# Kernel tuning notes

Measured on AMD Instinct MI355X. Metric: run time of the kernel, lower is better.

Reference implementation:

```python
import jax, jax.numpy as jnp
import numpy as np

D = 1024      # latent_dimension
NH = 8        # num_heads
ND = 256      # drug num_functions
NT = 128      # target num_functions
B = 128       # batch
EPS_LN = 1e-5
EPS_COS = 1e-8


def _proj_attend(x, W, b, in_w, in_b, out_w, out_b, g, beta):
    """ParallelFcWithAttention.forward: per-feature Linear(1,D)+ReLU, MHSA, LN, sum.
    x: (B, >=F); W,b: (F, D); in_w: (3D, D); out_w: (D, D); g,beta: (D,)."""
    F = W.shape[0]
    # fused batched scale+bias+ReLU replacing the Python loop of Linear(1,D)
    h = jax.nn.relu(x[:, :F, None] * W[None] + b[None])           # (B, F, D)
    Bsz = h.shape[0]
    qkv = h @ in_w.T + in_b                                       # (B, F, 3D)
    q, k, v = jnp.split(qkv, 3, axis=-1)
    Dh = D // NH
    def split_heads(t):
        return t.reshape(Bsz, F, NH, Dh).transpose(0, 2, 1, 3)   # (B, H, F, Dh)
    q, k, v = split_heads(q), split_heads(k), split_heads(v)
    scale = np.float32(1.0 / np.sqrt(Dh))
    scores = jnp.einsum('bhqd,bhkd->bhqk', q, k) * scale          # (B, H, F, F)
    attn = jax.nn.softmax(scores, axis=-1)
    o = jnp.einsum('bhqk,bhkd->bhqd', attn, v)                    # (B, H, F, Dh)
    o = o.transpose(0, 2, 1, 3).reshape(Bsz, F, D)
    o = o @ out_w.T + out_b
    mu = o.mean(axis=-1, keepdims=True)
    var = ((o - mu) ** 2).mean(axis=-1, keepdims=True)
    o = (o - mu) / jnp.sqrt(var + EPS_LN) * g + beta              # LayerNorm
    return o.sum(axis=1)                                          # (B, D)


def setup_inputs() -> dict:
    key = jax.random.key(0)
    ks = jax.random.split(key, 20)
    s = np.float32(0.02)
    inp = {
        'drug':    jax.random.normal(ks[0], (B, 2048), jnp.float32),
        'target':  jax.random.normal(ks[1], (B, 1024), jnp.float32),
        'dW':      jax.random.normal(ks[2], (ND, D), jnp.float32) * s,
        'db':      jax.random.normal(ks[3], (ND, D), jnp.float32) * s,
        'd_in_w':  jax.random.normal(ks[4], (3 * D, D), jnp.float32) * s,
        'd_in_b':  jnp.zeros((3 * D,), jnp.float32),
        'd_out_w': jax.random.normal(ks[5], (D, D), jnp.float32) * s,
        'd_out_b': jnp.zeros((D,), jnp.float32),
        'd_g':     jnp.ones((D,), jnp.float32),
        'd_beta':  jnp.zeros((D,), jnp.float32),
        'tW':      jax.random.normal(ks[6], (NT, D), jnp.float32) * s,
        'tb':      jax.random.normal(ks[7], (NT, D), jnp.float32) * s,
        't_in_w':  jax.random.normal(ks[8], (3 * D, D), jnp.float32) * s,
        't_in_b':  jnp.zeros((3 * D,), jnp.float32),
        't_out_w': jax.random.normal(ks[9], (D, D), jnp.float32) * s,
        't_out_b': jnp.zeros((D,), jnp.float32),
        't_g':     jnp.ones((D,), jnp.float32),
        't_beta':  jnp.zeros((D,), jnp.float32),
    }
    return inp


def reference(drug, target, dW, db, d_in_w, d_in_b, d_out_w, d_out_b, d_g, d_beta,
              tW, tb, t_in_w, t_in_b, t_out_w, t_out_b, t_g, t_beta):
    dp = _proj_attend(drug, dW, db, d_in_w, d_in_b, d_out_w, d_out_b, d_g, d_beta)   # (B, D)
    tp = _proj_attend(target, tW, tb, t_in_w, t_in_b, t_out_w, t_out_b, t_g, t_beta) # (B, D)
    # Cosine similarity over latent dim (torch CosineSimilarity dim=1), then sigmoid
    dot = jnp.sum(dp * tp, axis=-1)
    denom = jnp.maximum(jnp.linalg.norm(dp, axis=-1) * jnp.linalg.norm(tp, axis=-1), EPS_COS)
    return jax.nn.sigmoid(dot / denom)                                               # (B,)
```

## Files before the change

### kernel.cpp

```cpp
#include <hip/hip_runtime.h>

typedef unsigned short u16;
typedef unsigned int   u32;
typedef unsigned char  u8;

using bf16x8 = __attribute__((ext_vector_type(8))) short;
using f32x4  = __attribute__((ext_vector_type(4))) float;
using i32x4  = __attribute__((ext_vector_type(4))) int;

__device__ __forceinline__ float bf2f(u16 h) {
  u32 u = ((u32)h) << 16;
  return __builtin_bit_cast(float, u);
}
__device__ __forceinline__ u16 f2bf(float f) {
  u32 u = __builtin_bit_cast(u32, f);
  u += 0x7fffu + ((u >> 16) & 1u);
  return (u16)(u >> 16);
}

__device__ __forceinline__ void gload16(const void* src, void* ldsdst) {
  __builtin_amdgcn_global_load_lds(
      (const __attribute__((address_space(1))) void*)src,
      (__attribute__((address_space(3))) void*)ldsdst, 16, 0, 0);
}

__device__ __forceinline__ void mfma_i8(i32x4& c, i32x4 a, i32x4 b) {
  asm volatile("v_mfma_i32_16x16x64_i8 %0, %1, %2, %0" : "+a"(c) : "v"(a), "v"(b));
}

__device__ __forceinline__ int xcd_swz(int wg, int nwg) {
  int q = nwg >> 3, r = nwg & 7, xcd = wg & 7, loc = wg >> 3;
  return (xcd < r ? xcd * (q + 1) : r * (q + 1) + (xcd - r) * q) + loc;
}

__global__ __launch_bounds__(256) void cvt_w_i8(const float* __restrict__ in,
                                                u8* __restrict__ out,
                                                float* __restrict__ sc) {
  const int row  = blockIdx.x * 4 + (threadIdx.x >> 6);
  const int lane = threadIdx.x & 63;
  const float4* p = (const float4*)(in + (size_t)row * 1024 + lane * 16);
  float v[16];
  float mx = 0.f;
#pragma unroll
  for (int i = 0; i < 4; ++i) {
    float4 t = p[i];
    v[i * 4 + 0] = t.x; v[i * 4 + 1] = t.y; v[i * 4 + 2] = t.z; v[i * 4 + 3] = t.w;
#pragma unroll
    for (int j = 0; j < 4; ++j) mx = fmaxf(mx, fabsf(v[i * 4 + j]));
  }
#pragma unroll
  for (int m = 1; m < 64; m <<= 1) mx = fmaxf(mx, __shfl_xor(mx, m));
  const float scale = mx > 0.f ? 127.f / mx : 0.f;
  u32 pk[4];
#pragma unroll
  for (int i = 0; i < 4; ++i) {
    u32 b0 = (u32)(__float2int_rn(v[i * 4 + 0] * scale) & 0xff);
    u32 b1 = (u32)(__float2int_rn(v[i * 4 + 1] * scale) & 0xff);
    u32 b2 = (u32)(__float2int_rn(v[i * 4 + 2] * scale) & 0xff);
    u32 b3 = (u32)(__float2int_rn(v[i * 4 + 3] * scale) & 0xff);
    pk[i] = b0 | (b1 << 8) | (b2 << 16) | (b3 << 24);
  }
  *(uint4*)(out + (size_t)row * 1024 + lane * 16) = make_uint4(pk[0], pk[1], pk[2], pk[3]);
  if (lane == 0) sc[row] = mx > 0.f ? mx / 127.f : 0.f;
}

__global__ __launch_bounds__(256) void quant_i8(const u16* __restrict__ in,
                                                u8* __restrict__ out,
                                                float* __restrict__ sc) {
  const int row  = blockIdx.x * 4 + (threadIdx.x >> 6);
  const int lane = threadIdx.x & 63;
  const u16* p = in + (size_t)row * 1024 + lane * 16;
  float v[16];
  float mx = 0.f;
#pragma unroll
  for (int i = 0; i < 2; ++i) {
    bf16x8 t = *(const bf16x8*)(p + i * 8);
#pragma unroll
    for (int j = 0; j < 8; ++j) {
      float f = bf2f((u16)t[j]);
      v[i * 8 + j] = f;
      mx = fmaxf(mx, fabsf(f));
    }
  }
#pragma unroll
  for (int m = 1; m < 64; m <<= 1) mx = fmaxf(mx, __shfl_xor(mx, m));
  const float scale = mx > 0.f ? 127.f / mx : 0.f;
  u32 pk[4];
#pragma unroll
  for (int i = 0; i < 4; ++i) {
    u32 b0 = (u32)(__float2int_rn(v[i * 4 + 0] * scale) & 0xff);
    u32 b1 = (u32)(__float2int_rn(v[i * 4 + 1] * scale) & 0xff);
    u32 b2 = (u32)(__float2int_rn(v[i * 4 + 2] * scale) & 0xff);
    u32 b3 = (u32)(__float2int_rn(v[i * 4 + 3] * scale) & 0xff);
    pk[i] = b0 | (b1 << 8) | (b2 << 16) | (b3 << 24);
  }
  *(uint4*)(out + (size_t)row * 1024 + lane * 16) = make_uint4(pk[0], pk[1], pk[2], pk[3]);
  if (lane == 0) sc[row] = mx > 0.f ? mx / 127.f : 0.f;
}

__global__ __launch_bounds__(256) void hgen_i8(const float* __restrict__ x,
                                               const float* __restrict__ W,
                                               const float* __restrict__ bias,
                                               u8* __restrict__ h, float* __restrict__ hsc,
                                               int F, int logF, int b0, int xstride) {
  const int row  = blockIdx.x * 4 + (threadIdx.x >> 6);
  const int lane = threadIdx.x & 63;
  const int f = row & (F - 1);
  const int b = b0 + (row >> logF);
  const float xv = x[(size_t)b * xstride + f];
  const float4* wp = (const float4*)(W + (size_t)f * 1024 + lane * 16);
  const float4* bp = (const float4*)(bias + (size_t)f * 1024 + lane * 16);
  float hv[16];
  float mx = 0.f;
#pragma unroll
  for (int i = 0; i < 4; ++i) {
    float4 wv = wp[i];
    float4 bv = bp[i];
    hv[i * 4 + 0] = fmaxf(xv * wv.x + bv.x, 0.f);
    hv[i * 4 + 1] = fmaxf(xv * wv.y + bv.y, 0.f);
    hv[i * 4 + 2] = fmaxf(xv * wv.z + bv.z, 0.f);
    hv[i * 4 + 3] = fmaxf(xv * wv.w + bv.w, 0.f);
#pragma unroll
    for (int j = 0; j < 4; ++j) mx = fmaxf(mx, hv[i * 4 + j]);
  }
#pragma unroll
  for (int m = 1; m < 64; m <<= 1) mx = fmaxf(mx, __shfl_xor(mx, m));
  const float scale = mx > 0.f ? 127.f / mx : 0.f;
  u32 pk[4];
#pragma unroll
  for (int i = 0; i < 4; ++i) {
    u32 q0 = (u32)__float2int_rn(hv[i * 4 + 0] * scale);
    u32 q1 = (u32)__float2int_rn(hv[i * 4 + 1] * scale);
    u32 q2 = (u32)__float2int_rn(hv[i * 4 + 2] * scale);
    u32 q3 = (u32)__float2int_rn(hv[i * 4 + 3] * scale);
    pk[i] = q0 | (q1 << 8) | (q2 << 16) | (q3 << 24);
  }
  *(uint4*)(h + (size_t)row * 1024 + lane * 16) = make_uint4(pk[0], pk[1], pk[2], pk[3]);
  if (lane == 0) hsc[row] = mx > 0.f ? mx / 127.f : 0.f;
}

template <bool STATS>
__global__ __launch_bounds__(512, 4) void gemm_i8(const u8* __restrict__ A,
                                                  const u8* __restrict__ B,
                                                  const float* __restrict__ sAsc,
                                                  const float* __restrict__ sBsc,
                                                  const float* __restrict__ bias,
                                                  u16* __restrict__ C,
                                                  float2* __restrict__ stats,
                                                  int M, int N, int K) {
  __shared__ u8 sA[3][256 * 64];
  __shared__ u8 sB[3][128 * 64];
  const int tid  = threadIdx.x;
  const int lane = tid & 63;
  const int w    = tid >> 6;
  const int wm   = w >> 1;
  const int wn   = w & 1;

  const int nwg = gridDim.x * gridDim.y;
  const int wg  = blockIdx.y * gridDim.x + blockIdx.x;
  const int swz = xcd_swz(wg, nwg);
  const int n0 = (swz % gridDim.x) * 128;
  const int m0 = (swz / gridDim.x) * 256;

  i32x4 acc[4][4] = {};

  const int r_in  = lane >> 2;
  const int s_src = (lane & 3) ^ ((lane >> 3) & 3);

  auto stage = [&](int kt, int b) {
    const int k0 = kt << 6;
    gload16(A + (size_t)(m0 + w * 16 + r_in) * K + k0 + s_src * 16, &sA[b][w * 1024]);
    gload16(A + (size_t)(m0 + (w + 8) * 16 + r_in) * K + k0 + s_src * 16, &sA[b][(w + 8) * 1024]);
    gload16(B + (size_t)(n0 + w * 16 + r_in) * K + k0 + s_src * 16, &sB[b][w * 1024]);
  };

  const int NT = K >> 6;
  stage(0, 0);
  stage(1, 1);
  asm volatile("s_waitcnt vmcnt(3)" ::: "memory");
  __builtin_amdgcn_s_barrier();

  int cur = 0, nx = 2;
  for (int t = 0; t < NT; ++t) {
    const bool more = (t + 2 < NT);
    if (more) stage(t + 2, nx);

    i32x4 af[4], bg[4];
    const int g = lane >> 4;
#pragma unroll
    for (int mf = 0; mf < 4; ++mf) {
      int ra = wm * 64 + mf * 16 + (lane & 15);
      af[mf] = *(const i32x4*)(&sA[cur][ra * 64 + ((g ^ ((ra >> 1) & 3)) * 16)]);
    }
#pragma unroll
    for (int nf = 0; nf < 4; ++nf) {
      int rb = wn * 64 + nf * 16 + (lane & 15);
      bg[nf] = *(const i32x4*)(&sB[cur][rb * 64 + ((g ^ ((rb >> 1) & 3)) * 16)]);
    }
    asm volatile("s_waitcnt lgkmcnt(0)" ::: "memory");
    __builtin_amdgcn_sched_barrier(0);
    __builtin_amdgcn_s_setprio(1);
#pragma unroll
    for (int mf = 0; mf < 4; ++mf)
#pragma unroll
      for (int nf = 0; nf < 4; ++nf)
        mfma_i8(acc[mf][nf], af[mf], bg[nf]);
    __builtin_amdgcn_s_setprio(0);
    if (more) asm volatile("s_waitcnt vmcnt(3)" ::: "memory");
    else      asm volatile("s_waitcnt vmcnt(0)" ::: "memory");
    __builtin_amdgcn_s_barrier();
    cur = (cur == 2) ? 0 : cur + 1;
    nx  = (nx  == 2) ? 0 : nx  + 1;
  }

  float sb4[4], bs4[4];
#pragma unroll
  for (int nf = 0; nf < 4; ++nf) {
    int cl = n0 + wn * 64 + nf * 16 + (lane & 15);
    sb4[nf] = sBsc[cl];
    bs4[nf] = bias[cl];
  }
#pragma unroll
  for (int mf = 0; mf < 4; ++mf) {
    int r0 = m0 + wm * 64 + mf * 16 + (lane >> 4) * 4;
    float4 sa4 = *(const float4*)(sAsc + r0);
    const float* sap = (const float*)&sa4;
#pragma unroll
    for (int reg = 0; reg < 4; ++reg) {
      float s = 0.f, s2 = 0.f;
#pragma unroll
      for (int nf = 0; nf < 4; ++nf) {
        int cl = n0 + wn * 64 + nf * 16 + (lane & 15);
        float v = (float)acc[mf][nf][reg] * (sap[reg] * sb4[nf]) + bs4[nf];
        C[(size_t)(r0 + reg) * N + cl] = f2bf(v);
        if (STATS) { s += v; s2 += v * v; }
      }
      if (STATS) {
#pragma unroll
        for (int m = 1; m < 16; m <<= 1) { s += __shfl_xor(s, m); s2 += __shfl_xor(s2, m); }
        if ((lane & 15) == 0) {
          atomicAdd(&stats[r0 + reg].x, s);
          atomicAdd(&stats[r0 + reg].y, s2);
        }
      }
    }
  }
}

__global__ __launch_bounds__(256) void ln_fin(float2* __restrict__ stats, int n) {
  int i = blockIdx.x * 256 + threadIdx.x;
  if (i >= n) return;
  float2 s = stats[i];
  float mu  = s.x * (1.f / 1024.f);
  float var = s.y * (1.f / 1024.f) - mu * mu;
  stats[i] = make_float2(mu, rsqrtf(var + 1e-5f));
}

__global__ __launch_bounds__(1024, 1) void attn(const u16* __restrict__ qkv,
                                                u16* __restrict__ o_out, int F) {
  __shared__ u16 k_lds[64 * 136];
  __shared__ u16 vT[128 * 72];
  __shared__ u16 p_lds[16 * 16 * 72];

  const int tid  = threadIdx.x;
  const int lane = tid & 63;
  const int w    = tid >> 6;
  const int nt   = blockDim.x;

  const int head = blockIdx.x & 7;
  const int bc   = blockIdx.x >> 3;

  const size_t rowbase = (size_t)bc * F * 3072;
  const float scale = 0.12751744865678818f;

  const int qr = lane & 15;
  const int g4 = lane >> 4;

  bf16x8 qreg[4];
  {
    const u16* qsrc = qkv + rowbase + (size_t)(w * 16 + qr) * 3072 + head * 128;
#pragma unroll
    for (int kk = 0; kk < 4; ++kk) {
      bf16x8 v = *(const bf16x8*)(qsrc + kk * 32 + 8 * g4);
#pragma unroll
      for (int j = 0; j < 8; ++j) v[j] = (short)f2bf(bf2f((u16)v[j]) * scale);
      qreg[kk] = v;
    }
  }

  f32x4 o_acc[8] = {};
  float m_run = -INFINITY, l_run = 0.f;

  const int nkb = F >> 6;
  for (int kb = 0; kb < nkb; ++kb) {
    __syncthreads();
    const u16* ksrc = qkv + rowbase + (size_t)(kb * 64) * 3072 + 1024 + head * 128;
    const u16* vsrc = ksrc + 1024;
    for (int it = tid; it < 1024; it += nt) {
      int r = it >> 4, s = it & 15;
      *(bf16x8*)(k_lds + r * 136 + s * 8) = *(const bf16x8*)(ksrc + (size_t)r * 3072 + s * 8);
    }
    for (int it = tid; it < 512; it += nt) {
      int g2 = it >> 4, s = it & 15;
      const u16* v0 = vsrc + (size_t)(2 * g2) * 3072 + s * 8;
      bf16x8 a = *(const bf16x8*)(v0);
      bf16x8 b = *(const bf16x8*)(v0 + 3072);
      int rs0 = (2 * g2) ^ ((s & 7) << 3);
      int d0  = s * 8;
#pragma unroll
      for (int j = 0; j < 8; ++j) {
        u32 pk = (u32)(u16)a[j] | ((u32)(u16)b[j] << 16);
        *(u32*)(vT + (d0 + j) * 72 + rs0) = pk;
      }
    }
    __syncthreads();

    f32x4 sa[4] = {};
#pragma unroll
    for (int kk = 0; kk < 4; ++kk) {
#pragma unroll
      for (int f = 0; f < 4; ++f) {
        bf16x8 ak = *(const bf16x8*)(k_lds + (f * 16 + qr) * 136 + kk * 32 + 8 * g4);
        sa[f] = __builtin_amdgcn_mfma_f32_16x16x32_bf16(ak, qreg[kk], sa[f], 0, 0, 0);
      }
    }

    float tmax = -INFINITY;
#pragma unroll
    for (int f = 0; f < 4; ++f)
#pragma unroll
      for (int rr = 0; rr < 4; ++rr) tmax = fmaxf(tmax, sa[f][rr]);
    tmax = fmaxf(tmax, __shfl_xor(tmax, 16));
    tmax = fmaxf(tmax, __shfl_xor(tmax, 32));

    const bool ns = !__all(tmax - m_run <= 8.f);
    float mnew = m_run, alpha = 1.f;
    if (ns) { mnew = fmaxf(m_run, tmax); alpha = exp2f(m_run - mnew); }

    float psum = 0.f;
#pragma unroll
    for (int f = 0; f < 4; ++f) {
      u16 pp[4];
#pragma unroll
      for (int rr = 0; rr < 4; ++rr) {
        float p = exp2f(sa[f][rr] - mnew);
        psum += p;
        pp[rr] = f2bf(p);
      }
      uint2 u;
      u.x = (u32)pp[0] | ((u32)pp[1] << 16);
      u.y = (u32)pp[2] | ((u32)pp[3] << 16);
      *(uint2*)(p_lds + w * 1152 + qr * 72 + f * 16 + g4 * 4) = u;
    }
    psum += __shfl_xor(psum, 16);
    psum += __shfl_xor(psum, 32);
    l_run = l_run * alpha + psum;
    m_run = mnew;

    if (ns) {
#pragma unroll
      for (int rr = 0; rr < 4; ++rr) {
        float ar = __shfl(alpha, g4 * 4 + rr);
#pragma unroll
        for (int g = 0; g < 8; ++g) o_acc[g][rr] *= ar;
      }
    }

#pragma unroll
    for (int kk2 = 0; kk2 < 2; ++kk2) {
      bf16x8 pa = *(const bf16x8*)(p_lds + w * 1152 + qr * 72 + kk2 * 32 + 8 * g4);
#pragma unroll
      for (int g = 0; g < 8; ++g) {
        int swv = ((g * 2 + (qr >> 3)) & 7) << 3;
        bf16x8 vb = *(const bf16x8*)(vT + (g * 16 + qr) * 72 + ((kk2 * 32 + 8 * g4) ^ swv));
        o_acc[g] = __builtin_amdgcn_mfma_f32_16x16x32_bf16(pa, vb, o_acc[g], 0, 0, 0);
      }
    }
  }

  float linv = 1.f / l_run;
#pragma unroll
  for (int rr = 0; rr < 4; ++rr) {
    float lr = __shfl(linv, g4 * 4 + rr);
    size_t row = (size_t)bc * F + w * 16 + g4 * 4 + rr;
#pragma unroll
    for (int g = 0; g < 8; ++g)
      o_out[row * 1024 + head * 128 + g * 16 + qr] = f2bf(o_acc[g][rr] * lr);
  }
}

__global__ __launch_bounds__(256) void ln_accum(const u16* __restrict__ proj,
                                                const float2* __restrict__ stats,
                                                const float* __restrict__ g,
                                                const float* __restrict__ beta,
                                                float* __restrict__ dp, int F, int b0) {
  int d  = blockIdx.x * 256 + threadIdx.x;
  int bc = blockIdx.z;
  int f0 = blockIdx.y * 64;
  const u16* base = proj + ((size_t)(bc * F + f0)) * 1024 + d;
  const float2* st = stats + bc * F + f0;
  float acc = 0.f;
  for (int f = 0; f < 64; ++f) {
    float2 s = st[f];
    acc += (bf2f(base[(size_t)f * 1024]) - s.x) * s.y;
  }
  acc = acc * g[d] + 64.f * beta[d];
  atomicAdd(&dp[(size_t)(b0 + bc) * 1024 + d], acc);
}

__global__ __launch_bounds__(256) void cosine_sig(const float* __restrict__ dp,
                                                  const float* __restrict__ tp,
                                                  float* __restrict__ out) {
  __shared__ float red[3][4];
  int b = blockIdx.x;
  int tid = threadIdx.x, lane = tid & 63, w = tid >> 6;
  float dot = 0.f, n1 = 0.f, n2 = 0.f;
  for (int i = tid; i < 1024; i += 256) {
    float a = dp[(size_t)b * 1024 + i], c = tp[(size_t)b * 1024 + i];
    dot += a * c; n1 += a * a; n2 += c * c;
  }
#pragma unroll
  for (int m = 1; m < 64; m <<= 1) {
    dot += __shfl_xor(dot, m); n1 += __shfl_xor(n1, m); n2 += __shfl_xor(n2, m);
  }
  if (lane == 0) { red[0][w] = dot; red[1][w] = n1; red[2][w] = n2; }
  __syncthreads();
  if (tid == 0) {
    dot = red[0][0] + red[0][1] + red[0][2] + red[0][3];
    n1  = red[1][0] + red[1][1] + red[1][2] + red[1][3];
    n2  = red[2][0] + red[2][1] + red[2][2] + red[2][3];
    float denom = fmaxf(sqrtf(n1) * sqrtf(n2), 1e-8f);
    out[b] = 1.f / (1.f + __expf(-dot / denom));
  }
}

extern "C" void kernel_launch(void* const* d_in, const int* in_sizes, int n_in,
                              void* d_out, int out_size, void* d_ws, size_t ws_size,
                              hipStream_t stream) {
  const float* drug   = (const float*)d_in[0];
  const float* target = (const float*)d_in[1];

  char* p = (char*)d_ws;
  auto alloc = [&](size_t bytes) -> char* {
    char* r = p; p += (bytes + 255) & ~(size_t)255; return r;
  };

  u8*    w8_d    = (u8*)alloc((size_t)3072 * 1024);
  float* wsc_d   = (float*)alloc((size_t)3072 * 4);
  u8*    w8_t    = (u8*)alloc((size_t)3072 * 1024);
  float* wsc_t   = (float*)alloc((size_t)3072 * 4);
  u8*    w8o_d   = (u8*)alloc((size_t)1024 * 1024);
  float* wsco_d  = (float*)alloc((size_t)1024 * 4);
  u8*    w8o_t   = (u8*)alloc((size_t)1024 * 1024);
  float* wsco_t  = (float*)alloc((size_t)1024 * 4);
  float* dp      = (float*)alloc((size_t)2 * 128 * 1024 * 4);
  float* tp      = dp + 128 * 1024;

  size_t fixed = (size_t)(p - (char*)d_ws);
  size_t per = (size_t)256 * 1024
             + (size_t)256 * 4 + 256
             + (size_t)256 * 3072 * 2 + 256
             + (size_t)256 * 1024 * 2 + 256
             + (size_t)256 * 8 + 1024;
  int Bc = 8;
  if      (fixed + 128 * per <= ws_size) Bc = 128;
  else if (fixed +  96 * per <= ws_size) Bc = 96;
  else if (fixed +  64 * per <= ws_size) Bc = 64;
  else if (fixed +  32 * per <= ws_size) Bc = 32;
  else if (fixed +  16 * per <= ws_size) Bc = 16;

  u8*    h8     = (u8*)alloc((size_t)Bc * 256 * 1024);
  float* hsc    = (float*)alloc((size_t)Bc * 256 * 4);
  u16*   qkvbuf = (u16*)alloc((size_t)Bc * 256 * 3072 * 2);
  u16*   projbuf= qkvbuf;
  u16*   obuf   = (u16*)alloc((size_t)Bc * 256 * 1024 * 2);
  float2* statsb = (float2*)alloc((size_t)Bc * 256 * 8);

  cvt_w_i8<<<768, 256, 0, stream>>>((const float*)d_in[4],  w8_d, wsc_d);
  cvt_w_i8<<<768, 256, 0, stream>>>((const float*)d_in[12], w8_t, wsc_t);
  cvt_w_i8<<<256, 256, 0, stream>>>((const float*)d_in[6],  w8o_d, wsco_d);
  cvt_w_i8<<<256, 256, 0, stream>>>((const float*)d_in[14], w8o_t, wsco_t);
  hipMemsetAsync(dp, 0, (size_t)2 * 128 * 1024 * 4, stream);

  for (int br = 0; br < 2; ++br) {
    const int F = br ? 128 : 256, logF = br ? 7 : 8, xstride = br ? 1024 : 2048;
    const float* x    = br ? target : drug;
    const float* W    = (const float*)d_in[br ? 10 : 2];
    const float* Wb   = (const float*)d_in[br ? 11 : 3];
    u8*          w8   = br ? w8_t : w8_d;
    float*       wsc  = br ? wsc_t : wsc_d;
    const float* inb  = (const float*)d_in[br ? 13 : 5];
    u8*          w8o  = br ? w8o_t : w8o_d;
    float*       wsco = br ? wsco_t : wsco_d;
    const float* outb = (const float*)d_in[br ? 15 : 7];
    const float* gg   = (const float*)d_in[br ? 16 : 8];
    const float* bb   = (const float*)d_in[br ? 17 : 9];
    float*       accp = br ? tp : dp;

    const int nbmax = br ? (2 * Bc > 128 ? 128 : 2 * Bc) : (Bc > 128 ? 128 : Bc);

    for (int b0 = 0; b0 < 128; ) {
      int nb = nbmax;
      if (b0 + nb > 128) nb = 128 - b0;
      const int Mr = nb * F;
      hgen_i8<<<Mr / 4, 256, 0, stream>>>(x, W, Wb, h8, hsc, F, logF, b0, xstride);
      gemm_i8<false><<<dim3(3072 / 128, Mr / 256), 512, 0, stream>>>(
          h8, w8, hsc, wsc, inb, qkvbuf, nullptr, Mr, 3072, 1024);
      attn<<<8 * nb, 64 * (F / 16), 0, stream>>>(qkvbuf, obuf, F);
      quant_i8<<<Mr / 4, 256, 0, stream>>>(obuf, h8, hsc);
      hipMemsetAsync(statsb, 0, (size_t)Mr * 8, stream);
      gemm_i8<true><<<dim3(1024 / 128, Mr / 256), 512, 0, stream>>>(
          h8, w8o, hsc, wsco, outb, projbuf, statsb, Mr, 1024, 1024);
      ln_fin<<<(Mr + 255) / 256, 256, 0, stream>>>(statsb, Mr);
      ln_accum<<<dim3(4, F / 64, nb), 256, 0, stream>>>(projbuf, statsb, gg, bb, accp, F, b0);
      b0 += nb;
    }
  }
  cosine_sig<<<128, 256, 0, stream>>>(dp, tp, (float*)d_out);
}
```

Baseline: 543.8 us.

## Prefetch next K/V tile in registers, fold LN finalize, balance batch chunks

The attention kernel becomes templated on thread count and prefetches the next K/V block into registers while computing the current one. This overlaps global loads with MFMA work at the cost of extra registers. The separate ln_fin kernel is removed and its mean/rstd computation is folded into ln_accum, dropping one launch but repeating rsqrt work per element. Batch chunking is rebalanced so all chunks are about equal in size, avoiding a small trailing chunk.

```diff
diff --git a/kernel.cpp b/kernel.cpp
--- a/kernel.cpp
+++ b/kernel.cpp
@@ -247,17 +247,9 @@
   }
 }
 
-__global__ __launch_bounds__(256) void ln_fin(float2* __restrict__ stats, int n) {
-  int i = blockIdx.x * 256 + threadIdx.x;
-  if (i >= n) return;
-  float2 s = stats[i];
-  float mu  = s.x * (1.f / 1024.f);
-  float var = s.y * (1.f / 1024.f) - mu * mu;
-  stats[i] = make_float2(mu, rsqrtf(var + 1e-5f));
-}
-
-__global__ __launch_bounds__(1024, 1) void attn(const u16* __restrict__ qkv,
-                                                u16* __restrict__ o_out, int F) {
+template <int NT>
+__global__ __launch_bounds__(NT, 1) void attn(const u16* __restrict__ qkv,
+                                              u16* __restrict__ o_out, int F) {
   __shared__ u16 k_lds[64 * 136];
   __shared__ u16 vT[128 * 72];
   __shared__ u16 p_lds[16 * 16 * 72];
@@ -265,7 +257,6 @@
   const int tid  = threadIdx.x;
   const int lane = tid & 63;
   const int w    = tid >> 6;
-  const int nt   = blockDim.x;
 
   const int head = blockIdx.x & 7;
   const int bc   = blockIdx.x >> 3;
@@ -288,32 +279,56 @@
     }
   }
 
+  bf16x8 kreg[2], va[2], vb[2];
+  auto load_kv = [&](int kb) {
+    const u16* ksrc = qkv + rowbase + (size_t)(kb * 64) * 3072 + 1024 + head * 128;
+    const u16* vsrc = ksrc + 1024;
+#pragma unroll
+    for (int i = 0; i < 2; ++i) {
+      int it = tid + i * NT;
+      if (it < 1024) {
+        int r = it >> 4, s = it & 15;
+        kreg[i] = *(const bf16x8*)(ksrc + (size_t)r * 3072 + s * 8);
+      }
+      if (it < 512) {
+        int g2 = it >> 4, s = it & 15;
+        const u16* v0 = vsrc + (size_t)(2 * g2) * 3072 + s * 8;
+        va[i] = *(const bf16x8*)(v0);
+        vb[i] = *(const bf16x8*)(v0 + 3072);
+      }
+    }
+  };
+  auto store_kv = [&]() {
+#pragma unroll
+    for (int i = 0; i < 2; ++i) {
+      int it = tid + i * NT;
+      if (it < 1024) {
+        int r = it >> 4, s = it & 15;
+        *(bf16x8*)(k_lds + r * 136 + s * 8) = kreg[i];
+      }
+      if (it < 512) {
+        int g2 = it >> 4, s = it & 15;
+        int rs0 = (2 * g2) ^ ((s & 7) << 3);
+        int d0  = s * 8;
+#pragma unroll
+        for (int j = 0; j < 8; ++j) {
+          u32 pk = (u32)(u16)va[i][j] | ((u32)(u16)vb[i][j] << 16);
+          *(u32*)(vT + (d0 + j) * 72 + rs0) = pk;
+        }
+      }
+    }
+  };
+
   f32x4 o_acc[8] = {};
   float m_run = -INFINITY, l_run = 0.f;
 
+  load_kv(0);
   const int nkb = F >> 6;
   for (int kb = 0; kb < nkb; ++kb) {
     __syncthreads();
-    const u16* ksrc = qkv + rowbase + (size_t)(kb * 64) * 3072 + 1024 + head * 128;
-    const u16* vsrc = ksrc + 1024;
-    for (int it = tid; it < 1024; it += nt) {
-      int r = it >> 4, s = it & 15;
-      *(bf16x8*)(k_lds + r * 136 + s * 8) = *(const bf16x8*)(ksrc + (size_t)r * 3072 + s * 8);
-    }
-    for (int it = tid; it < 512; it += nt) {
-      int g2 = it >> 4, s = it & 15;
-      const u16* v0 = vsrc + (size_t)(2 * g2) * 3072 + s * 8;
-      bf16x8 a = *(const bf16x8*)(v0);
-      bf16x8 b = *(const bf16x8*)(v0 + 3072);
-      int rs0 = (2 * g2) ^ ((s & 7) << 3);
-      int d0  = s * 8;
-#pragma unroll
-      for (int j = 0; j < 8; ++j) {
-        u32 pk = (u32)(u16)a[j] | ((u32)(u16)b[j] << 16);
-        *(u32*)(vT + (d0 + j) * 72 + rs0) = pk;
-      }
-    }
+    store_kv();
     __syncthreads();
+    if (kb + 1 < nkb) load_kv(kb + 1);
 
     f32x4 sa[4] = {};
 #pragma unroll
@@ -372,8 +387,8 @@
 #pragma unroll
       for (int g = 0; g < 8; ++g) {
         int swv = ((g * 2 + (qr >> 3)) & 7) << 3;
-        bf16x8 vb = *(const bf16x8*)(vT + (g * 16 + qr) * 72 + ((kk2 * 32 + 8 * g4) ^ swv));
-        o_acc[g] = __builtin_amdgcn_mfma_f32_16x16x32_bf16(pa, vb, o_acc[g], 0, 0, 0);
+        bf16x8 vb2 = *(const bf16x8*)(vT + (g * 16 + qr) * 72 + ((kk2 * 32 + 8 * g4) ^ swv));
+        o_acc[g] = __builtin_amdgcn_mfma_f32_16x16x32_bf16(pa, vb2, o_acc[g], 0, 0, 0);
       }
     }
   }
@@ -402,7 +417,9 @@
   float acc = 0.f;
   for (int f = 0; f < 64; ++f) {
     float2 s = st[f];
-    acc += (bf2f(base[(size_t)f * 1024]) - s.x) * s.y;
+    float mu  = s.x * (1.f / 1024.f);
+    float var = s.y * (1.f / 1024.f) - mu * mu;
+    acc += (bf2f(base[(size_t)f * 1024]) - mu) * rsqrtf(var + 1e-5f);
   }
   acc = acc * g[d] + 64.f * beta[d];
   atomicAdd(&dp[(size_t)(b0 + bc) * 1024 + d], acc);
@@ -498,20 +515,23 @@
     float*       accp = br ? tp : dp;
 
     const int nbmax = br ? (2 * Bc > 128 ? 128 : 2 * Bc) : (Bc > 128 ? 128 : Bc);
+    const int nch   = (128 + nbmax - 1) / nbmax;
+    int nb0 = (128 + nch - 1) / nch;
+    if (br) nb0 = (nb0 + 1) & ~1;
 
     for (int b0 = 0; b0 < 128; ) {
-      int nb = nbmax;
+      int nb = nb0;
       if (b0 + nb > 128) nb = 128 - b0;
       const int Mr = nb * F;
       hgen_i8<<<Mr / 4, 256, 0, stream>>>(x, W, Wb, h8, hsc, F, logF, b0, xstride);
       gemm_i8<false><<<dim3(3072 / 128, Mr / 256), 512, 0, stream>>>(
           h8, w8, hsc, wsc, inb, qkvbuf, nullptr, Mr, 3072, 1024);
-      attn<<<8 * nb, 64 * (F / 16), 0, stream>>>(qkvbuf, obuf, F);
+      if (br) attn<512><<<8 * nb, 512, 0, stream>>>(qkvbuf, obuf, F);
+      else    attn<1024><<<8 * nb, 1024, 0, stream>>>(qkvbuf, obuf, F);
       quant_i8<<<Mr / 4, 256, 0, stream>>>(obuf, h8, hsc);
       hipMemsetAsync(statsb, 0, (size_t)Mr * 8, stream);
       gemm_i8<true><<<dim3(1024 / 128, Mr / 256), 512, 0, stream>>>(
           h8, w8o, hsc, wsco, outb, projbuf, statsb, Mr, 1024, 1024);
-      ln_fin<<<(Mr + 255) / 256, 256, 0, stream>>>(statsb, Mr);
       ln_accum<<<dim3(4, F / 64, nb), 256, 0, stream>>>(projbuf, statsb, gg, bb, accp, F, b0);
       b0 += nb;
     }
```

New measurement: 535.2 us. No clear change (-1.6%).
